# Optimization experiments

Measured on AMD Instinct MI355X. Metric: run time of the kernel, lower is better.

The kernel has to match this reference:

```python
import jax, jax.numpy as jnp
import numpy as np

E, H, I = 8, 2048, 4096  # num_experts, hidden_size, intermediate_size
B, K = 2048, 2           # batch_seq tokens, top_k


def setup_inputs() -> dict:
    key = jax.random.key(0)
    k_x, k_idx, k_w, k1, k2, k3 = jax.random.split(key, 6)
    # kaiming-uniform-ish init for expert weights
    bound1 = float(np.sqrt(6.0 / H))
    bound2 = float(np.sqrt(6.0 / I))
    return {
        "x": jax.random.normal(k_x, (B, H), dtype=jnp.float32),
        "expert_indices": jax.random.randint(k_idx, (B, K), 0, E, dtype=jnp.int64),
        "expert_weights": jax.random.uniform(k_w, (B, K), dtype=jnp.float32),
        "w1": jax.random.uniform(k1, (E, H, I), dtype=jnp.float32, minval=-bound1, maxval=bound1),
        "w2": jax.random.uniform(k2, (E, I, H), dtype=jnp.float32, minval=-bound2, maxval=bound2),
        "w3": jax.random.uniform(k3, (E, H, I), dtype=jnp.float32, minval=-bound1, maxval=bound1),
    }


def reference(x, expert_indices, expert_weights, w1, w2, w3):
    # Same math as the torch module (per-token top-k SwiGLU MoE), but computed
    # as dense per-expert GEMMs + output gather instead of materializing
    # per-token gathered weight slices (which would be B*K*H*I elements).
    gate = jax.nn.silu(jnp.einsum('bh,ehi->bei', x, w1))   # [B,E,I]
    up = jnp.einsum('bh,ehi->bei', x, w3)                  # [B,E,I]
    out_all = jnp.einsum('bei,eih->beh', gate * up, w2)    # [B,E,H]
    # select the top_k experts' outputs per token
    sel = jnp.take_along_axis(out_all, expert_indices[:, :, None], axis=1)  # [B,K,H]
    return (sel * expert_weights[:, :, None]).sum(axis=1)  # [B,H]
```

## Files before the change

### kernel.cpp

```cpp
#include <hip/hip_runtime.h>

#define EXPERTS 8
#define HID 2048
#define INTER 4096
#define BTOK 2048
#define NASSIGN 4096
#define NTSLOTS 40

typedef float f32x4 __attribute__((ext_vector_type(4)));
typedef __bf16 bf16x8 __attribute__((ext_vector_type(8)));
typedef unsigned short ushortx8 __attribute__((ext_vector_type(8)));

__device__ __forceinline__ unsigned short f2bf(float f) {
  union { float f; unsigned int u; } v; v.f = f;
  unsigned int r = v.u + 0x7fffu + ((v.u >> 16) & 1u);
  return (unsigned short)(r >> 16);
}

#define XB_OFF   0ULL
#define GB_OFF   (XB_OFF + 8388608ULL)
#define Y_OFF    (GB_OFF + 33554432ULL)
#define ROWS_OFF (Y_OFF  + 33554432ULL)
#define OFFS_OFF (ROWS_OFF + 16384ULL)
#define TILE_OFF (OFFS_OFF + 64ULL)

__global__ void prep_kernel(const int* __restrict__ eraw,
                            const float* __restrict__ x,
                            unsigned short* __restrict__ xb,
                            int* __restrict__ rows, int* __restrict__ offs_g,
                            int* __restrict__ tiles)
{
  const int b = blockIdx.x;
  const int tid = threadIdx.x;

  if (b == 0) {
    __shared__ int cnt[256 * 8];
    __shared__ int offs_s[9];
    __shared__ int tot[8];
    __shared__ int found_odd;
    if (tid == 0) found_odd = 0;
    __syncthreads();
    int any = 0;
    for (int j = 0; j < 8; ++j) {
      int a = tid * 8 + j;
      any |= (eraw[2 * a + 1] != 0);
    }
    if (any) atomicOr(&found_odd, 1);
    __syncthreads();
    const bool i64 = (found_odd == 0);
    int lc[8];
    for (int e = 0; e < 8; ++e) lc[e] = 0;
    for (int j = 0; j < 16; ++j) {
      int a = tid * 16 + j;
      int e = i64 ? eraw[2 * a] : eraw[a];
      lc[e]++;
    }
    for (int e = 0; e < 8; ++e) cnt[tid * 8 + e] = lc[e];
    __syncthreads();
    if (tid < 8) {
      int run = 0;
      for (int t = 0; t < 256; ++t) {
        int v = cnt[t * 8 + tid];
        cnt[t * 8 + tid] = run;
        run += v;
      }
      tot[tid] = run;
    }
    __syncthreads();
    if (tid == 0) {
      int o = 0;
      for (int e = 0; e < 8; ++e) { offs_s[e] = o; o += tot[e]; }
      offs_s[8] = o;
      int s = 0;
      for (int e = 0; e < 8; ++e) {
        int nmt = (tot[e] + 127) >> 7;
        for (int m = 0; m < nmt; ++m) tiles[s++] = (e << 16) | m;
      }
      for (; s < NTSLOTS; ++s) tiles[s] = -1;
    }
    __syncthreads();
    if (tid < 9) offs_g[tid] = offs_s[tid];
    int lc2[8];
    for (int e = 0; e < 8; ++e) lc2[e] = 0;
    for (int j = 0; j < 16; ++j) {
      int a = tid * 16 + j;
      int e = i64 ? eraw[2 * a] : eraw[a];
      rows[offs_s[e] + cnt[tid * 8 + e] + lc2[e]] = a;
      lc2[e]++;
    }
  } else {
    long idx = (long)(b - 1) * 256 + tid;
    float4 v = *(const float4*)&x[idx * 4];
    unsigned int lo = (unsigned int)f2bf(v.x) | ((unsigned int)f2bf(v.y) << 16);
    unsigned int hi = (unsigned int)f2bf(v.z) | ((unsigned int)f2bf(v.w) << 16);
    uint2 p; p.x = lo; p.y = hi;
    *(uint2*)&xb[idx * 4] = p;
  }
}

__global__ __launch_bounds__(256, 4) void gemm_gateup(
    const unsigned short* __restrict__ xb,
    const float* __restrict__ w1,
    const float* __restrict__ w3,
    unsigned short* __restrict__ gb,
    const int* __restrict__ rows,
    const int* __restrict__ offs,
    const int* __restrict__ tiles)
{
  const int te = tiles[blockIdx.y];
  if (te < 0) return;
  const int e  = te >> 16, mt = te & 0xffff;
  const int off = offs[e];
  const int cnt = offs[e + 1] - off;
  const int nt  = blockIdx.x;

  __shared__ __align__(16) unsigned short As[2][128 * 32];
  __shared__ __align__(16) unsigned short B1bf[2][4 * 64 * 8];
  __shared__ __align__(16) unsigned short B3bf[2][4 * 64 * 8];

  const int tid  = threadIdx.x;
  const int lane = tid & 63;
  const int wave = tid >> 6;
  const int wr = wave >> 1, wc = wave & 1;

  const unsigned short* aptr[2];
  #pragma unroll
  for (int c = 0; c < 2; ++c) {
    int idx = tid + c * 256;
    int row = idx >> 2, seg = idx & 3;
    int rr = off + mt * 128 + row;
    int rv = (rr < off + cnt) ? rr : (off + cnt - 1);
    long tok = rows[rv] >> 1;
    aptr[c] = xb + tok * HID + seg * 8;
  }
  const int bn = tid & 63, bk8 = tid >> 6;
  const float* b1base = w1 + ((long)e * HID + bk8 * 8) * INTER + nt * 64 + bn;
  const float* b3base = w3 + ((long)e * HID + bk8 * 8) * INTER + nt * 64 + bn;

  auto STAGE_A = [&](int abuf, long k32) {
    #pragma unroll
    for (int c = 0; c < 2; ++c)
      __builtin_amdgcn_global_load_lds(
          (const __attribute__((address_space(1))) unsigned int*)(aptr[c] + k32),
          (__attribute__((address_space(3))) unsigned int*)(&As[abuf][(tid + c * 256) * 8]),
          16, 0, 0);
  };

  float rB1[8], rB3[8];
  auto LOAD_B = [&](int t) {
    const float* p1 = b1base + (long)t * 32 * INTER;
    const float* p3 = b3base + (long)t * 32 * INTER;
    #pragma unroll
    for (int j = 0; j < 8; ++j) {
      rB1[j] = p1[(long)j * INTER];
      rB3[j] = p3[(long)j * INTER];
    }
  };

  f32x4 acc1[4][2], acc3[4][2];
  #pragma unroll
  for (int i = 0; i < 4; ++i)
    #pragma unroll
    for (int j = 0; j < 2; ++j) { acc1[i][j] = (f32x4)0.0f; acc3[i][j] = (f32x4)0.0f; }

  LOAD_B(0);
  STAGE_A(0, 0);

  const int NIT = HID / 32;
  for (int t = 0; t < NIT; ++t) {
    const int p = t & 1;
    {
      bf16x8 p1, p3;
      #pragma unroll
      for (int j = 0; j < 8; ++j) {
        p1[j] = (__bf16)rB1[j];
        p3[j] = (__bf16)rB3[j];
      }
      *(bf16x8*)&B1bf[p][(bk8 * 64 + bn) * 8] = p1;
      *(bf16x8*)&B3bf[p][(bk8 * 64 + bn) * 8] = p3;
    }
    if (t + 1 < NIT) LOAD_B(t + 1);
    __syncthreads();
    if (t + 1 < NIT) STAGE_A((t + 1) & 1, (long)(t + 1) * 32);
    const int k8 = lane >> 4;
    bf16x8 af[4], b1f[2], b3f[2];
    #pragma unroll
    for (int f = 0; f < 4; ++f)
      af[f] = __builtin_bit_cast(bf16x8, *(const ushortx8*)&As[p][(wr * 64 + f * 16 + (lane & 15)) * 32 + k8 * 8]);
    #pragma unroll
    for (int j = 0; j < 2; ++j) {
      b1f[j] = __builtin_bit_cast(bf16x8, *(const ushortx8*)&B1bf[p][(k8 * 64 + wc * 32 + j * 16 + (lane & 15)) * 8]);
      b3f[j] = __builtin_bit_cast(bf16x8, *(const ushortx8*)&B3bf[p][(k8 * 64 + wc * 32 + j * 16 + (lane & 15)) * 8]);
    }
    #pragma unroll
    for (int i = 0; i < 4; ++i)
      #pragma unroll
      for (int j = 0; j < 2; ++j) {
        acc1[i][j] = __builtin_amdgcn_mfma_f32_16x16x32_bf16(af[i], b1f[j], acc1[i][j], 0, 0, 0);
        acc3[i][j] = __builtin_amdgcn_mfma_f32_16x16x32_bf16(af[i], b3f[j], acc3[i][j], 0, 0, 0);
      }
  }

  const int rtop = off + cnt;
  const int grb  = off + mt * 128 + wr * 64;
  const int gcb  = nt * 64 + wc * 32;
  #pragma unroll
  for (int i = 0; i < 4; ++i) {
    #pragma unroll
    for (int j = 0; j < 2; ++j) {
      int gc = gcb + j * 16 + (lane & 15);
      #pragma unroll
      for (int qq = 0; qq < 4; ++qq) {
        int gr = grb + i * 16 + (lane >> 4) * 4 + qq;
        if (gr < rtop) {
          float g = acc1[i][j][qq];
          float u = acc3[i][j][qq];
          float s = g / (1.0f + __expf(-g));
          gb[(long)gr * INTER + gc] = f2bf(s * u);
        }
      }
    }
  }
}

__global__ __launch_bounds__(256, 4) void gemm_down(
    const unsigned short* __restrict__ gbin,
    const float* __restrict__ w2,
    float* __restrict__ y,
    const int* __restrict__ rows,
    const int* __restrict__ offs,
    const int* __restrict__ tiles)
{
  const int te = tiles[blockIdx.y];
  if (te < 0) return;
  const int e  = te >> 16, mt = te & 0xffff;
  const int off = offs[e];
  const int cnt = offs[e + 1] - off;
  const int nt  = blockIdx.x;

  __shared__ __align__(16) unsigned short As[2][128 * 32];
  __shared__ __align__(16) unsigned short Bbf[2][4 * 64 * 8];

  const int tid  = threadIdx.x;
  const int lane = tid & 63;
  const int wave = tid >> 6;
  const int wr = wave >> 1, wc = wave & 1;

  const unsigned short* aptr[2];
  #pragma unroll
  for (int c = 0; c < 2; ++c) {
    int idx = tid + c * 256;
    int row = idx >> 2, seg = idx & 3;
    int rr = off + mt * 128 + row;
    int rv = (rr < off + cnt) ? rr : (off + cnt - 1);
    aptr[c] = gbin + (long)rv * INTER + seg * 8;
  }
  const int bn = tid & 63, bk8 = tid >> 6;
  const float* bbase = w2 + ((long)e * INTER + bk8 * 8) * HID + nt * 64 + bn;

  auto STAGE_A = [&](int abuf, long k32) {
    #pragma unroll
    for (int c = 0; c < 2; ++c)
      __builtin_amdgcn_global_load_lds(
          (const __attribute__((address_space(1))) unsigned int*)(aptr[c] + k32),
          (__attribute__((address_space(3))) unsigned int*)(&As[abuf][(tid + c * 256) * 8]),
          16, 0, 0);
  };

  float rB[8];
  auto LOAD_B = [&](int t) {
    const float* p = bbase + (long)t * 32 * HID;
    #pragma unroll
    for (int j = 0; j < 8; ++j) rB[j] = p[(long)j * HID];
  };

  f32x4 acc[4][2];
  #pragma unroll
  for (int i = 0; i < 4; ++i)
    #pragma unroll
    for (int j = 0; j < 2; ++j) acc[i][j] = (f32x4)0.0f;

  LOAD_B(0);
  STAGE_A(0, 0);

  const int NIT = INTER / 32;
  for (int t = 0; t < NIT; ++t) {
    const int p = t & 1;
    {
      bf16x8 pk;
      #pragma unroll
      for (int j = 0; j < 8; ++j) pk[j] = (__bf16)rB[j];
      *(bf16x8*)&Bbf[p][(bk8 * 64 + bn) * 8] = pk;
    }
    if (t + 1 < NIT) LOAD_B(t + 1);
    __syncthreads();
    if (t + 1 < NIT) STAGE_A((t + 1) & 1, (long)(t + 1) * 32);
    const int k8 = lane >> 4;
    bf16x8 af[4], bf[2];
    #pragma unroll
    for (int f = 0; f < 4; ++f)
      af[f] = __builtin_bit_cast(bf16x8, *(const ushortx8*)&As[p][(wr * 64 + f * 16 + (lane & 15)) * 32 + k8 * 8]);
    #pragma unroll
    for (int j = 0; j < 2; ++j)
      bf[j] = __builtin_bit_cast(bf16x8, *(const ushortx8*)&Bbf[p][(k8 * 64 + wc * 32 + j * 16 + (lane & 15)) * 8]);
    #pragma unroll
    for (int i = 0; i < 4; ++i)
      #pragma unroll
      for (int j = 0; j < 2; ++j)
        acc[i][j] = __builtin_amdgcn_mfma_f32_16x16x32_bf16(af[i], bf[j], acc[i][j], 0, 0, 0);
  }

  const int rtop = off + cnt;
  const int grb  = off + mt * 128 + wr * 64;
  const int gcb  = nt * 64 + wc * 32;
  #pragma unroll
  for (int i = 0; i < 4; ++i) {
    #pragma unroll
    for (int j = 0; j < 2; ++j) {
      int gc = gcb + j * 16 + (lane & 15);
      #pragma unroll
      for (int q = 0; q < 4; ++q) {
        int gr = grb + i * 16 + (lane >> 4) * 4 + q;
        if (gr < rtop) {
          int a = rows[gr];
          y[(long)a * HID + gc] = acc[i][j][q];
        }
      }
    }
  }
}

__global__ void combine_kernel(const float* __restrict__ Y,
                               const float* __restrict__ ew,
                               float* __restrict__ out)
{
  int idx = blockIdx.x * 256 + threadIdx.x;
  int t = idx >> 9;
  int h = (idx & 511) * 4;
  float w0 = ew[2 * t], w1 = ew[2 * t + 1];
  float4 y0 = *(const float4*)&Y[(long)(2 * t) * HID + h];
  float4 y1 = *(const float4*)&Y[(long)(2 * t + 1) * HID + h];
  float4 o;
  o.x = w0 * y0.x + w1 * y1.x;
  o.y = w0 * y0.y + w1 * y1.y;
  o.z = w0 * y0.z + w1 * y1.z;
  o.w = w0 * y0.w + w1 * y1.w;
  *(float4*)&out[(long)t * HID + h] = o;
}

extern "C" void kernel_launch(void* const* d_in, const int* in_sizes, int n_in,
                              void* d_out, int out_size, void* d_ws, size_t ws_size,
                              hipStream_t stream) {
  const float* x   = (const float*)d_in[0];
  const int*   eix = (const int*)d_in[1];
  const float* ew  = (const float*)d_in[2];
  const float* w1  = (const float*)d_in[3];
  const float* w2  = (const float*)d_in[4];
  const float* w3  = (const float*)d_in[5];
  float* out = (float*)d_out;

  char* ws = (char*)d_ws;
  unsigned short* xb  = (unsigned short*)(ws + XB_OFF);
  unsigned short* gb  = (unsigned short*)(ws + GB_OFF);
  float*          y   = (float*)(ws + Y_OFF);
  int*            rows  = (int*)(ws + ROWS_OFF);
  int*            offs  = (int*)(ws + OFFS_OFF);
  int*            tiles = (int*)(ws + TILE_OFF);

  prep_kernel<<<4097, 256, 0, stream>>>(eix, x, xb, rows, offs, tiles);
  gemm_gateup<<<dim3(INTER / 64, NTSLOTS), 256, 0, stream>>>(
      xb, w1, w3, gb, rows, offs, tiles);
  gemm_down<<<dim3(HID / 64, NTSLOTS), 256, 0, stream>>>(
      gb, w2, y, rows, offs, tiles);
  combine_kernel<<<4096, 256, 0, stream>>>(y, ew, out);
}
```

Measured before the change: 480.8 us.

## Double MoE GEMM row tile to 256 with 512-thread blocks

Both expert GEMMs now process 256 token rows per block using 8 waves instead of 128 rows with 4 waves, which halves the number of row tiles per expert and the tile slot count. Each block's fp32 weight tile is fetched and converted to bf16 once for twice as many rows, cutting repeated weight reads from global memory. In gate/up, the w1 and w3 loads are split across the two halves of the block. In down, only the first half of the block loads weights. The trade-offs are larger blocks, more LDS, more register pressure under the new launch bounds, and more padded rows for experts whose token count is not a multiple of 256.

```diff
diff --git a/kernel.cpp b/kernel.cpp
--- a/kernel.cpp
+++ b/kernel.cpp
@@ -5,7 +5,7 @@
 #define INTER 4096
 #define BTOK 2048
 #define NASSIGN 4096
-#define NTSLOTS 40
+#define NTSLOTS 24
 
 typedef float f32x4 __attribute__((ext_vector_type(4)));
 typedef __bf16 bf16x8 __attribute__((ext_vector_type(8)));
@@ -73,7 +73,7 @@
       offs_s[8] = o;
       int s = 0;
       for (int e = 0; e < 8; ++e) {
-        int nmt = (tot[e] + 127) >> 7;
+        int nmt = (tot[e] + 255) >> 8;
         for (int m = 0; m < nmt; ++m) tiles[s++] = (e << 16) | m;
       }
       for (; s < NTSLOTS; ++s) tiles[s] = -1;
@@ -98,7 +98,7 @@
   }
 }
 
-__global__ __launch_bounds__(256, 4) void gemm_gateup(
+__global__ __launch_bounds__(512, 4) void gemm_gateup(
     const unsigned short* __restrict__ xb,
     const float* __restrict__ w1,
     const float* __restrict__ w3,
@@ -114,7 +114,7 @@
   const int cnt = offs[e + 1] - off;
   const int nt  = blockIdx.x;
 
-  __shared__ __align__(16) unsigned short As[2][128 * 32];
+  __shared__ __align__(16) unsigned short As[2][256 * 32];
   __shared__ __align__(16) unsigned short B1bf[2][4 * 64 * 8];
   __shared__ __align__(16) unsigned short B3bf[2][4 * 64 * 8];
 
@@ -126,35 +126,33 @@
   const unsigned short* aptr[2];
   #pragma unroll
   for (int c = 0; c < 2; ++c) {
-    int idx = tid + c * 256;
+    int idx = tid + c * 512;
     int row = idx >> 2, seg = idx & 3;
-    int rr = off + mt * 128 + row;
+    int rr = off + mt * 256 + row;
     int rv = (rr < off + cnt) ? rr : (off + cnt - 1);
     long tok = rows[rv] >> 1;
     aptr[c] = xb + tok * HID + seg * 8;
   }
-  const int bn = tid & 63, bk8 = tid >> 6;
-  const float* b1base = w1 + ((long)e * HID + bk8 * 8) * INTER + nt * 64 + bn;
-  const float* b3base = w3 + ((long)e * HID + bk8 * 8) * INTER + nt * 64 + bn;
+  const int bslot = tid & 255;
+  const int bn = bslot & 63, bk8 = bslot >> 6;
+  const bool isB1 = (tid < 256);
+  const float* wsel = isB1 ? w1 : w3;
+  const float* bbase = wsel + ((long)e * HID + bk8 * 8) * INTER + nt * 64 + bn;
 
   auto STAGE_A = [&](int abuf, long k32) {
     #pragma unroll
     for (int c = 0; c < 2; ++c)
       __builtin_amdgcn_global_load_lds(
           (const __attribute__((address_space(1))) unsigned int*)(aptr[c] + k32),
-          (__attribute__((address_space(3))) unsigned int*)(&As[abuf][(tid + c * 256) * 8]),
+          (__attribute__((address_space(3))) unsigned int*)(&As[abuf][(tid + c * 512) * 8]),
           16, 0, 0);
   };
 
-  float rB1[8], rB3[8];
+  float rB[8];
   auto LOAD_B = [&](int t) {
-    const float* p1 = b1base + (long)t * 32 * INTER;
-    const float* p3 = b3base + (long)t * 32 * INTER;
-    #pragma unroll
-    for (int j = 0; j < 8; ++j) {
-      rB1[j] = p1[(long)j * INTER];
-      rB3[j] = p3[(long)j * INTER];
-    }
+    const float* p = bbase + (long)t * 32 * INTER;
+    #pragma unroll
+    for (int j = 0; j < 8; ++j) rB[j] = p[(long)j * INTER];
   };
 
   f32x4 acc1[4][2], acc3[4][2];
@@ -170,14 +168,11 @@
   for (int t = 0; t < NIT; ++t) {
     const int p = t & 1;
     {
-      bf16x8 p1, p3;
-      #pragma unroll
-      for (int j = 0; j < 8; ++j) {
-        p1[j] = (__bf16)rB1[j];
-        p3[j] = (__bf16)rB3[j];
-      }
-      *(bf16x8*)&B1bf[p][(bk8 * 64 + bn) * 8] = p1;
-      *(bf16x8*)&B3bf[p][(bk8 * 64 + bn) * 8] = p3;
+      bf16x8 pk;
+      #pragma unroll
+      for (int j = 0; j < 8; ++j) pk[j] = (__bf16)rB[j];
+      if (isB1) *(bf16x8*)&B1bf[p][(bk8 * 64 + bn) * 8] = pk;
+      else      *(bf16x8*)&B3bf[p][(bk8 * 64 + bn) * 8] = pk;
     }
     if (t + 1 < NIT) LOAD_B(t + 1);
     __syncthreads();
@@ -202,7 +197,7 @@
   }
 
   const int rtop = off + cnt;
-  const int grb  = off + mt * 128 + wr * 64;
+  const int grb  = off + mt * 256 + wr * 64;
   const int gcb  = nt * 64 + wc * 32;
   #pragma unroll
   for (int i = 0; i < 4; ++i) {
@@ -223,7 +218,7 @@
   }
 }
 
-__global__ __launch_bounds__(256, 4) void gemm_down(
+__global__ __launch_bounds__(512, 4) void gemm_down(
     const unsigned short* __restrict__ gbin,
     const float* __restrict__ w2,
     float* __restrict__ y,
@@ -238,7 +233,7 @@
   const int cnt = offs[e + 1] - off;
   const int nt  = blockIdx.x;
 
-  __shared__ __align__(16) unsigned short As[2][128 * 32];
+  __shared__ __align__(16) unsigned short As[2][256 * 32];
   __shared__ __align__(16) unsigned short Bbf[2][4 * 64 * 8];
 
   const int tid  = threadIdx.x;
@@ -249,13 +244,15 @@
   const unsigned short* aptr[2];
   #pragma unroll
   for (int c = 0; c < 2; ++c) {
-    int idx = tid + c * 256;
+    int idx = tid + c * 512;
     int row = idx >> 2, seg = idx & 3;
-    int rr = off + mt * 128 + row;
+    int rr = off + mt * 256 + row;
     int rv = (rr < off + cnt) ? rr : (off + cnt - 1);
     aptr[c] = gbin + (long)rv * INTER + seg * 8;
   }
-  const int bn = tid & 63, bk8 = tid >> 6;
+  const int bslot = tid & 255;
+  const int bn = bslot & 63, bk8 = bslot >> 6;
+  const bool doB = (tid < 256);
   const float* bbase = w2 + ((long)e * INTER + bk8 * 8) * HID + nt * 64 + bn;
 
   auto STAGE_A = [&](int abuf, long k32) {
@@ -263,15 +260,17 @@
     for (int c = 0; c < 2; ++c)
       __builtin_amdgcn_global_load_lds(
           (const __attribute__((address_space(1))) unsigned int*)(aptr[c] + k32),
-          (__attribute__((address_space(3))) unsigned int*)(&As[abuf][(tid + c * 256) * 8]),
+          (__attribute__((address_space(3))) unsigned int*)(&As[abuf][(tid + c * 512) * 8]),
           16, 0, 0);
   };
 
   float rB[8];
   auto LOAD_B = [&](int t) {
-    const float* p = bbase + (long)t * 32 * HID;
-    #pragma unroll
-    for (int j = 0; j < 8; ++j) rB[j] = p[(long)j * HID];
+    if (doB) {
+      const float* p = bbase + (long)t * 32 * HID;
+      #pragma unroll
+      for (int j = 0; j < 8; ++j) rB[j] = p[(long)j * HID];
+    }
   };
 
   f32x4 acc[4][2];
@@ -286,7 +285,7 @@
   const int NIT = INTER / 32;
   for (int t = 0; t < NIT; ++t) {
     const int p = t & 1;
-    {
+    if (doB) {
       bf16x8 pk;
       #pragma unroll
       for (int j = 0; j < 8; ++j) pk[j] = (__bf16)rB[j];
@@ -311,7 +310,7 @@
   }
 
   const int rtop = off + cnt;
-  const int grb  = off + mt * 128 + wr * 64;
+  const int grb  = off + mt * 256 + wr * 64;
   const int gcb  = nt * 64 + wc * 32;
   #pragma unroll
   for (int i = 0; i < 4; ++i) {
@@ -368,9 +367,9 @@
   int*            tiles = (int*)(ws + TILE_OFF);
 
   prep_kernel<<<4097, 256, 0, stream>>>(eix, x, xb, rows, offs, tiles);
-  gemm_gateup<<<dim3(INTER / 64, NTSLOTS), 256, 0, stream>>>(
+  gemm_gateup<<<dim3(INTER / 64, NTSLOTS), 512, 0, stream>>>(
       xb, w1, w3, gb, rows, offs, tiles);
-  gemm_down<<<dim3(HID / 64, NTSLOTS), 256, 0, stream>>>(
+  gemm_down<<<dim3(HID / 64, NTSLOTS), 512, 0, stream>>>(
       gb, w2, y, rows, offs, tiles);
   combine_kernel<<<4096, 256, 0, stream>>>(y, ew, out);
 }
```

Result: faster. 455.6 us (-5.2%).
